# Performance work log

Measured on AMD Instinct MI355X. Metric: run time of the kernel, lower is better.

## Reference

```python
import jax, jax.numpy as jnp
import numpy as np

B, H, D, STEP = 2048, 512, 256, 64  # batch, context_size (cell), thetas_dim (proj/input), steps


def setup_inputs() -> dict:
    key = jax.random.key(0)
    ks = jax.random.split(key, 6)
    s = 1.0 / np.sqrt(H)  # PyTorch LSTM init scale
    c = jax.random.normal(ks[0], (B, H, 1), jnp.float32)
    W_ih = jax.random.uniform(ks[1], (4 * H, D), jnp.float32, -s, s)
    W_hh = jax.random.uniform(ks[2], (4 * H, D), jnp.float32, -s, s)  # hidden input is projected -> dim D
    b_ih = jax.random.uniform(ks[3], (4 * H,), jnp.float32, -s, s)
    b_hh = jax.random.uniform(ks[4], (4 * H,), jnp.float32, -s, s)
    W_hr = jax.random.uniform(ks[5], (D, H), jnp.float32, -s, s)  # projection weight (proj_size=D)
    return {"c": c, "W_ih": W_ih, "W_hh": W_hh, "b_ih": b_ih, "b_hh": b_hh, "W_hr": W_hr, "step": STEP}


def reference(c, W_ih, W_hh, b_ih, b_hh, W_hr, step):
    # c: [batch, hidden, num_layers=1] -> initial cell state [batch, hidden]
    batch = c.shape[0]
    d = W_ih.shape[1]
    c0 = c[:, :, 0]
    h0 = jnp.zeros((batch, d), c.dtype)  # x0 == h0 == 0; thereafter fed-back input x equals projected h

    def cell(carry, _):
        h, cc = carry
        # gates: input term (x==h) + hidden term, PyTorch order i,f,g,o
        z = h @ W_ih.T + b_ih + h @ W_hh.T + b_hh  # [batch, 4H]
        i, f, g, o = jnp.split(z, 4, axis=-1)
        i = jax.nn.sigmoid(i)
        f = jax.nn.sigmoid(f)
        g = jnp.tanh(g)
        o = jax.nn.sigmoid(o)
        cc = f * cc + i * g
        h_new = (o * jnp.tanh(cc)) @ W_hr.T  # projection to proj_size=D
        return (h_new, cc), h_new

    _, ys = jax.lax.scan(cell, (h0, c0), None, length=step)  # ys: [step, batch, D]
    return jnp.transpose(ys, (1, 2, 0))  # [batch, thetas_dim, step]
```

## Files before the change

### kernel.cpp

```cpp
#include <hip/hip_runtime.h>
#include <cstdint>
#include <cstddef>

constexpr int NB  = 2048;
constexpr int NH  = 512;
constexpr int ND  = 256;
constexpr int NT  = 64;
constexpr int N4H = 2048;

typedef __attribute__((ext_vector_type(8))) __bf16 bf16x8;
typedef __attribute__((ext_vector_type(4))) float  f32x4;

__device__ inline unsigned short f2bf_rne(float f) {
    unsigned u = __builtin_bit_cast(unsigned, f);
    unsigned r = (u + 0x7FFFu + ((u >> 16) & 1u)) >> 16;
    return (unsigned short)r;
}
__device__ inline float bf2f(unsigned short h) {
    unsigned u = ((unsigned)h) << 16;
    return __builtin_bit_cast(float, u);
}

__global__ __launch_bounds__(256) void prep_kernel(
    const float* __restrict__ c,   const float* __restrict__ Wih,
    const float* __restrict__ Whh, const float* __restrict__ bih,
    const float* __restrict__ bhh, const float* __restrict__ Whr,
    float* __restrict__ cc, float* __restrict__ bsum,
    unsigned short* __restrict__ WrH,  unsigned short* __restrict__ WrL,
    unsigned short* __restrict__ WhrH, unsigned short* __restrict__ WhrL,
    unsigned short* __restrict__ hH,   unsigned short* __restrict__ hL)
{
    int i = blockIdx.x * 256 + threadIdx.x;
    cc[i] = c[i];
    if (i < N4H) bsum[i] = bih[i] + bhh[i];
    if (i < N4H * ND) {
        int np = i >> 8, k = i & 255;
        int jg = np >> 7, r = np & 127, g = r >> 5, cu = r & 31;
        int src = (g * NH + jg * 32 + cu) * ND + k;
        float w = Wih[src] + Whh[src];
        unsigned short hi = f2bf_rne(w);
        WrH[i] = hi; WrL[i] = f2bf_rne(w - bf2f(hi));
        hH[i] = 0; hL[i] = 0;
    }
    if (i < ND * NH) {
        float w = Whr[i];
        unsigned short hi = f2bf_rne(w);
        WhrH[i] = hi; WhrL[i] = f2bf_rne(w - bf2f(hi));
    }
}

template <int ROWS>
__device__ __forceinline__ void stage_tile(const unsigned short* __restrict__ g,
                                           int row0, int ldgElems, int k0Elems,
                                           char* smem, int ldsOff, int wave, int lane)
{
    constexpr int QN = ROWS / 32;
#pragma unroll
    for (int q = 0; q < QN; ++q) {
        int L   = wave * (ROWS * 32) + q * 1024 + lane * 16;
        int row = L >> 7;
        int kb  = L & 127;
        int kbs = kb ^ ((row & 7) << 4);
        const char* src = (const char*)g +
            (size_t)(row0 + row) * (ldgElems * 2) + k0Elems * 2 + kbs;
        char* dst = smem + ldsOff + wave * (ROWS * 32) + q * 1024;
        __builtin_amdgcn_global_load_lds(
            (const __attribute__((address_space(1))) unsigned int*)src,
            (__attribute__((address_space(3))) unsigned int*)dst,
            16, 0, 0);
    }
}

__device__ __forceinline__ bf16x8 frag_ld(const char* smem, int off, int row, int kb) {
    int kbs = kb ^ ((row & 7) << 4);
    return *(const bf16x8*)(smem + off + row * 128 + kbs);
}

__global__ __launch_bounds__(256) void gates_step(
    const unsigned short* __restrict__ hH, const unsigned short* __restrict__ hL,
    const unsigned short* __restrict__ WrH, const unsigned short* __restrict__ WrL,
    const float* __restrict__ bsum, float* __restrict__ cc,
    unsigned short* __restrict__ aH, unsigned short* __restrict__ aL)
{
    __shared__ char smem[49152];
    constexpr int AsH = 0, AsL = 8192, BsH = 16384, BsL = 32768;

    const int tid  = threadIdx.x;
    const int lane = tid & 63;
    const int wave = tid >> 6;
    const int wr = wave >> 1, wc = wave & 1;
    const int b0 = blockIdx.x * 64;
    const int ny = blockIdx.y;
    const int n0 = ny * 128;

    f32x4 acc[2][4];
#pragma unroll
    for (int mi = 0; mi < 2; ++mi)
#pragma unroll
        for (int ni = 0; ni < 4; ++ni)
            acc[mi][ni] = f32x4{0.f, 0.f, 0.f, 0.f};

    const int lrow = lane & 15;
    const int lk   = (lane >> 4) * 16;

#pragma unroll 1
    for (int ch = 0; ch < 4; ++ch) {
        __syncthreads();
        stage_tile<64> (hH,  b0, ND, ch * 64, smem, AsH, wave, lane);
        stage_tile<64> (hL,  b0, ND, ch * 64, smem, AsL, wave, lane);
        stage_tile<128>(WrH, n0, ND, ch * 64, smem, BsH, wave, lane);
        stage_tile<128>(WrL, n0, ND, ch * 64, smem, BsL, wave, lane);
        __syncthreads();
#pragma unroll
        for (int kk = 0; kk < 2; ++kk) {
            const int kb = kk * 64 + lk;
            bf16x8 aHf[2], aLf[2], bHf[4], bLf[4];
#pragma unroll
            for (int mi = 0; mi < 2; ++mi) {
                int row = wr * 32 + mi * 16 + lrow;
                aHf[mi] = frag_ld(smem, AsH, row, kb);
                aLf[mi] = frag_ld(smem, AsL, row, kb);
            }
#pragma unroll
            for (int ni = 0; ni < 4; ++ni) {
                int row = wc * 64 + ni * 16 + lrow;
                bHf[ni] = frag_ld(smem, BsH, row, kb);
                bLf[ni] = frag_ld(smem, BsL, row, kb);
            }
#pragma unroll
            for (int mi = 0; mi < 2; ++mi)
#pragma unroll
                for (int ni = 0; ni < 4; ++ni) {
                    acc[mi][ni] = __builtin_amdgcn_mfma_f32_16x16x32_bf16(aHf[mi], bHf[ni], acc[mi][ni], 0, 0, 0);
                    acc[mi][ni] = __builtin_amdgcn_mfma_f32_16x16x32_bf16(aHf[mi], bLf[ni], acc[mi][ni], 0, 0, 0);
                    acc[mi][ni] = __builtin_amdgcn_mfma_f32_16x16x32_bf16(aLf[mi], bHf[ni], acc[mi][ni], 0, 0, 0);
                }
        }
    }
    __syncthreads();
    float (*z)[128] = (float(*)[128])smem;
#pragma unroll
    for (int mi = 0; mi < 2; ++mi)
#pragma unroll
        for (int ni = 0; ni < 4; ++ni)
#pragma unroll
            for (int r = 0; r < 4; ++r) {
                int m = wr * 32 + mi * 16 + (lane >> 4) * 4 + r;
                int n = wc * 64 + ni * 16 + (lane & 15);
                z[m][n] = acc[mi][ni][r];
            }
    __syncthreads();
    const int cu = tid & 31;
    const int rg = tid >> 5;
    const int j  = ny * 32 + cu;
    const float bi = bsum[0 * NH + j], bfv = bsum[1 * NH + j];
    const float bg = bsum[2 * NH + j], bo  = bsum[3 * NH + j];
#pragma unroll
    for (int it = 0; it < 8; ++it) {
        int m = rg * 8 + it;
        size_t idx = (size_t)(b0 + m) * NH + j;
        float zi = z[m][cu]      + bi;
        float zf = z[m][32 + cu] + bfv;
        float zg = z[m][64 + cu] + bg;
        float zo = z[m][96 + cu] + bo;
        float iv = 1.f / (1.f + expf(-zi));
        float fv = 1.f / (1.f + expf(-zf));
        float gv = tanhf(zg);
        float ov = 1.f / (1.f + expf(-zo));
        float cv = fv * cc[idx] + iv * gv;
        cc[idx] = cv;
        float av = ov * tanhf(cv);
        unsigned short ah = f2bf_rne(av);
        aH[idx] = ah;
        aL[idx] = f2bf_rne(av - bf2f(ah));
    }
}

template <bool STAGED>
__global__ __launch_bounds__(256) void recur_step(
    const unsigned short* __restrict__ aH, const unsigned short* __restrict__ aL,
    const unsigned short* __restrict__ WhrHp, const unsigned short* __restrict__ WhrLp,
    unsigned short* __restrict__ hH, unsigned short* __restrict__ hL,
    float* __restrict__ hseq, float* __restrict__ out, int t)
{
    __shared__ char smem[16384];
    constexpr int AsH = 0, AsL = 4096, BsH = 8192, BsL = 12288;

    const int tid  = threadIdx.x;
    const int lane = tid & 63;
    const int wave = tid >> 6;
    const int wr = wave >> 1, wc = wave & 1;
    const int b0 = blockIdx.x * 32;
    const int d0 = blockIdx.y * 32;

    f32x4 acc = f32x4{0.f, 0.f, 0.f, 0.f};

    const int lrow = lane & 15;
    const int lk   = (lane >> 4) * 16;

#pragma unroll 1
    for (int ch = 0; ch < 8; ++ch) {
        __syncthreads();
        stage_tile<32>(aH,    b0, NH, ch * 64, smem, AsH, wave, lane);
        stage_tile<32>(aL,    b0, NH, ch * 64, smem, AsL, wave, lane);
        stage_tile<32>(WhrHp, d0, NH, ch * 64, smem, BsH, wave, lane);
        stage_tile<32>(WhrLp, d0, NH, ch * 64, smem, BsL, wave, lane);
        __syncthreads();
#pragma unroll
        for (int kk = 0; kk < 2; ++kk) {
            const int kb = kk * 64 + lk;
            int arow = wr * 16 + lrow;
            int brow = wc * 16 + lrow;
            bf16x8 aHf = frag_ld(smem, AsH, arow, kb);
            bf16x8 aLf = frag_ld(smem, AsL, arow, kb);
            bf16x8 bHf = frag_ld(smem, BsH, brow, kb);
            bf16x8 bLf = frag_ld(smem, BsL, brow, kb);
            acc = __builtin_amdgcn_mfma_f32_16x16x32_bf16(aHf, bHf, acc, 0, 0, 0);
            acc = __builtin_amdgcn_mfma_f32_16x16x32_bf16(aHf, bLf, acc, 0, 0, 0);
            acc = __builtin_amdgcn_mfma_f32_16x16x32_bf16(aLf, bHf, acc, 0, 0, 0);
        }
    }
#pragma unroll
    for (int r = 0; r < 4; ++r) {
        int b = b0 + wr * 16 + (lane >> 4) * 4 + r;
        int d = d0 + wc * 16 + (lane & 15);
        float v = acc[r];
        if (STAGED) hseq[((size_t)t * NB + b) * ND + d] = v;
        else        out[((size_t)b * ND + d) * NT + t]  = v;
        size_t hidx = (size_t)b * ND + d;
        unsigned short hh = f2bf_rne(v);
        hH[hidx] = hh;
        hL[hidx] = f2bf_rne(v - bf2f(hh));
    }
}

__global__ __launch_bounds__(256) void transpose_kernel(
    const float* __restrict__ hseq, float* __restrict__ out) {
    __shared__ float tile[64][65];
    const int tid = threadIdx.x;
    const int d0  = blockIdx.x * 64;
    const int b   = blockIdx.y;
    const int x   = tid & 63;
    const int y   = tid >> 6;
#pragma unroll
    for (int r = 0; r < 16; ++r) {
        int t = y + r * 4;
        tile[t][x] = hseq[((size_t)t * NB + b) * ND + d0 + x];
    }
    __syncthreads();
#pragma unroll
    for (int r = 0; r < 16; ++r) {
        int d = y + r * 4;
        out[((size_t)b * ND + d0 + d) * NT + x] = tile[x][d];
    }
}

extern "C" void kernel_launch(void* const* d_in, const int* in_sizes, int n_in,
                              void* d_out, int out_size, void* d_ws, size_t ws_size,
                              hipStream_t stream) {
    const float* c   = (const float*)d_in[0];
    const float* Wih = (const float*)d_in[1];
    const float* Whh = (const float*)d_in[2];
    const float* bih = (const float*)d_in[3];
    const float* bhh = (const float*)d_in[4];
    const float* Whr = (const float*)d_in[5];
    float* out = (float*)d_out;

    char* ws = (char*)d_ws;
    size_t off = 0;
    auto alloc = [&](size_t bytes) -> char* {
        char* p = ws + off;
        off = (off + bytes + 255) & ~(size_t)255;
        return p;
    };
    float*          cc    = (float*)alloc((size_t)NB * NH * 4);
    float*          bsum  = (float*)alloc((size_t)N4H * 4);
    unsigned short* WrHp  = (unsigned short*)alloc((size_t)N4H * ND * 2);
    unsigned short* WrLp  = (unsigned short*)alloc((size_t)N4H * ND * 2);
    unsigned short* WhrHp = (unsigned short*)alloc((size_t)ND * NH * 2);
    unsigned short* WhrLp = (unsigned short*)alloc((size_t)ND * NH * 2);
    unsigned short* hH    = (unsigned short*)alloc((size_t)NB * ND * 2);
    unsigned short* hL    = (unsigned short*)alloc((size_t)NB * ND * 2);
    unsigned short* aH    = (unsigned short*)alloc((size_t)NB * NH * 2);
    unsigned short* aL    = (unsigned short*)alloc((size_t)NB * NH * 2);
    size_t hseq_bytes = (size_t)NT * NB * ND * 4;
    float* hseq = (float*)(ws + off);
    const bool staged = (off + hseq_bytes) <= ws_size;

    prep_kernel<<<(NB * NH) / 256, 256, 0, stream>>>(
        c, Wih, Whh, bih, bhh, Whr, cc, bsum, WrHp, WrLp, WhrHp, WhrLp, hH, hL);

    dim3 g1(NB / 64, N4H / 128);
    dim3 g2(NB / 32, ND / 32);
    for (int t = 0; t < NT; ++t) {
        gates_step<<<g1, 256, 0, stream>>>(hH, hL, WrHp, WrLp, bsum, cc, aH, aL);
        if (staged)
            recur_step<true><<<g2, 256, 0, stream>>>(aH, aL, WhrHp, WhrLp,
                                                     hH, hL, hseq, out, t);
        else
            recur_step<false><<<g2, 256, 0, stream>>>(aH, aL, WhrHp, WhrLp,
                                                      hH, hL, hseq, out, t);
    }
    if (staged) {
        dim3 gt(ND / 64, NB);
        transpose_kernel<<<gt, 256, 0, stream>>>(hseq, out);
    }
}
```

Measured before the change: 1.504 ms.

## Fold projection weight into gate weights and batch the output projection across steps

Precomputes W_big = (W_ih+W_hh)·W_hr once, so each step's gates are computed directly from the previous step's pre-projection activation. This leaves one kernel per step instead of two. Every step's activation is kept in a sequence buffer, and the projection to the outputs runs once as a single batched GEMM over all steps. The aim is to halve per-step launches and serial dependencies. The cost is that the per-step gate GEMM grows from K=256 to K=512, plus a large activation history buffer.

```diff
diff --git a/kernel.cpp b/kernel.cpp
--- a/kernel.cpp
+++ b/kernel.cpp
@@ -7,6 +7,7 @@
 constexpr int ND  = 256;
 constexpr int NT  = 64;
 constexpr int N4H = 2048;
+constexpr size_t SLOT = (size_t)NB * NH;
 
 typedef __attribute__((ext_vector_type(8))) __bf16 bf16x8;
 typedef __attribute__((ext_vector_type(4))) float  f32x4;
@@ -21,32 +22,87 @@
     return __builtin_bit_cast(float, u);
 }
 
-__global__ __launch_bounds__(256) void prep_kernel(
+__global__ __launch_bounds__(256) void prep1_kernel(
     const float* __restrict__ c,   const float* __restrict__ Wih,
     const float* __restrict__ Whh, const float* __restrict__ bih,
     const float* __restrict__ bhh, const float* __restrict__ Whr,
     float* __restrict__ cc, float* __restrict__ bsum,
-    unsigned short* __restrict__ WrH,  unsigned short* __restrict__ WrL,
+    float* __restrict__ Wsum_reord,
     unsigned short* __restrict__ WhrH, unsigned short* __restrict__ WhrL,
-    unsigned short* __restrict__ hH,   unsigned short* __restrict__ hL)
+    unsigned short* __restrict__ aHseq, unsigned short* __restrict__ aLseq)
 {
     int i = blockIdx.x * 256 + threadIdx.x;
     cc[i] = c[i];
+    aHseq[i] = 0; aLseq[i] = 0;
     if (i < N4H) bsum[i] = bih[i] + bhh[i];
     if (i < N4H * ND) {
         int np = i >> 8, k = i & 255;
         int jg = np >> 7, r = np & 127, g = r >> 5, cu = r & 31;
         int src = (g * NH + jg * 32 + cu) * ND + k;
-        float w = Wih[src] + Whh[src];
-        unsigned short hi = f2bf_rne(w);
-        WrH[i] = hi; WrL[i] = f2bf_rne(w - bf2f(hi));
-        hH[i] = 0; hL[i] = 0;
+        Wsum_reord[i] = Wih[src] + Whh[src];
     }
     if (i < ND * NH) {
         float w = Whr[i];
         unsigned short hi = f2bf_rne(w);
         WhrH[i] = hi; WhrL[i] = f2bf_rne(w - bf2f(hi));
     }
+}
+
+__global__ __launch_bounds__(256) void prep2_kernel(
+    const float* __restrict__ Wsum_reord, const float* __restrict__ Whr,
+    unsigned short* __restrict__ WbigH, unsigned short* __restrict__ WbigL)
+{
+    __shared__ float a_s[64][65];
+    __shared__ float b_s[64][68];
+    const int tid = threadIdx.x;
+    const int n0 = blockIdx.x * 64;
+    const int h0 = blockIdx.y * 64;
+    const int r  = tid >> 2;
+    const int q  = tid & 3;
+    const int tn = (tid & 15) * 4;
+    const int th = (tid >> 4) * 4;
+
+    float acc[4][4] = {};
+#pragma unroll 1
+    for (int ch = 0; ch < 4; ++ch) {
+        __syncthreads();
+#pragma unroll
+        for (int e = 0; e < 4; ++e) {
+            float4 v = *reinterpret_cast<const float4*>(
+                &Wsum_reord[(size_t)(n0 + r) * ND + ch * 64 + q * 16 + e * 4]);
+            int k = q * 16 + e * 4;
+            a_s[k + 0][r] = v.x; a_s[k + 1][r] = v.y;
+            a_s[k + 2][r] = v.z; a_s[k + 3][r] = v.w;
+        }
+#pragma unroll
+        for (int e = 0; e < 4; ++e) {
+            float4 v = *reinterpret_cast<const float4*>(
+                &Whr[(size_t)(ch * 64 + r) * NH + h0 + q * 16 + e * 4]);
+            *reinterpret_cast<float4*>(&b_s[r][q * 16 + e * 4]) = v;
+        }
+        __syncthreads();
+#pragma unroll 8
+        for (int k = 0; k < 64; ++k) {
+            float av[4], bv[4];
+#pragma unroll
+            for (int e = 0; e < 4; ++e) { av[e] = a_s[k][tn + e]; bv[e] = b_s[k][th + e]; }
+#pragma unroll
+            for (int ii = 0; ii < 4; ++ii)
+#pragma unroll
+                for (int jj = 0; jj < 4; ++jj)
+                    acc[ii][jj] += av[ii] * bv[jj];
+        }
+    }
+#pragma unroll
+    for (int ii = 0; ii < 4; ++ii)
+#pragma unroll
+        for (int jj = 0; jj < 4; ++jj) {
+            float w = acc[ii][jj];
+            unsigned short hi = f2bf_rne(w);
+            size_t idx = (size_t)(n0 + tn + ii) * NH + h0 + th + jj;
+            WbigH[idx] = hi;
+            WbigL[idx] = f2bf_rne(w - bf2f(hi));
+        }
 }
 
 template <int ROWS>
@@ -76,15 +132,13 @@
     return *(const bf16x8*)(smem + off + row * 128 + kbs);
 }
 
-__global__ __launch_bounds__(256) void gates_step(
-    const unsigned short* __restrict__ hH, const unsigned short* __restrict__ hL,
-    const unsigned short* __restrict__ WrH, const unsigned short* __restrict__ WrL,
-    const float* __restrict__ bsum, float* __restrict__ cc,
-    unsigned short* __restrict__ aH, unsigned short* __restrict__ aL)
+__global__ __launch_bounds__(256) void step_kernel(
+    const unsigned short* __restrict__ aHseq, const unsigned short* __restrict__ aLseq,
+    const unsigned short* __restrict__ WbigH, const unsigned short* __restrict__ WbigL,
+    const float* __restrict__ bsum, float* __restrict__ cc, int t)
 {
     __shared__ char smem[49152];
     constexpr int AsH = 0, AsL = 8192, BsH = 16384, BsL = 32768;
-
     const int tid  = threadIdx.x;
     const int lane = tid & 63;
     const int wave = tid >> 6;
@@ -93,6 +147,9 @@
     const int ny = blockIdx.y;
     const int n0 = ny * 128;
 
+    const unsigned short* aH = aHseq + (size_t)t * SLOT;
+    const unsigned short* aL = aLseq + (size_t)t * SLOT;
+
     f32x4 acc[2][4];
 #pragma unroll
     for (int mi = 0; mi < 2; ++mi)
@@ -104,12 +161,12 @@
     const int lk   = (lane >> 4) * 16;
 
 #pragma unroll 1
-    for (int ch = 0; ch < 4; ++ch) {
-        __syncthreads();
-        stage_tile<64> (hH,  b0, ND, ch * 64, smem, AsH, wave, lane);
-        stage_tile<64> (hL,  b0, ND, ch * 64, smem, AsL, wave, lane);
-        stage_tile<128>(WrH, n0, ND, ch * 64, smem, BsH, wave, lane);
-        stage_tile<128>(WrL, n0, ND, ch * 64, smem, BsL, wave, lane);
+    for (int ch = 0; ch < 8; ++ch) {
+        __syncthreads();
+        stage_tile<64> (aH,    b0, NH, ch * 64, smem, AsH, wave, lane);
+        stage_tile<64> (aL,    b0, NH, ch * 64, smem, AsL, wave, lane);
+        stage_tile<128>(WbigH, n0, NH, ch * 64, smem, BsH, wave, lane);
+        stage_tile<128>(WbigL, n0, NH, ch * 64, smem, BsL, wave, lane);
         __syncthreads();
 #pragma unroll
         for (int kk = 0; kk < 2; ++kk) {
@@ -155,6 +212,8 @@
     const int j  = ny * 32 + cu;
     const float bi = bsum[0 * NH + j], bfv = bsum[1 * NH + j];
     const float bg = bsum[2 * NH + j], bo  = bsum[3 * NH + j];
+    unsigned short* aHo = (unsigned short*)aHseq + (size_t)(t + 1) * SLOT;
+    unsigned short* aLo = (unsigned short*)aLseq + (size_t)(t + 1) * SLOT;
 #pragma unroll
     for (int it = 0; it < 8; ++it) {
         int m = rg * 8 + it;
@@ -171,29 +230,36 @@
         cc[idx] = cv;
         float av = ov * tanhf(cv);
         unsigned short ah = f2bf_rne(av);
-        aH[idx] = ah;
-        aL[idx] = f2bf_rne(av - bf2f(ah));
-    }
-}
-
-template <bool STAGED>
-__global__ __launch_bounds__(256) void recur_step(
-    const unsigned short* __restrict__ aH, const unsigned short* __restrict__ aL,
-    const unsigned short* __restrict__ WhrHp, const unsigned short* __restrict__ WhrLp,
-    unsigned short* __restrict__ hH, unsigned short* __restrict__ hL,
-    float* __restrict__ hseq, float* __restrict__ out, int t)
-{
-    __shared__ char smem[16384];
-    constexpr int AsH = 0, AsL = 4096, BsH = 8192, BsL = 12288;
-
+        aHo[idx] = ah;
+        aLo[idx] = f2bf_rne(av - bf2f(ah));
+    }
+}
+
+template <bool DIRECT>
+__global__ __launch_bounds__(256) void y_kernel(
+    const unsigned short* __restrict__ aHseq, const unsigned short* __restrict__ aLseq,
+    const unsigned short* __restrict__ WhrH, const unsigned short* __restrict__ WhrL,
+    float* __restrict__ hseq, float* __restrict__ out)
+{
+    __shared__ char smem[49152];
+    constexpr int AsH = 0, AsL = 8192, BsH = 16384, BsL = 32768;
     const int tid  = threadIdx.x;
     const int lane = tid & 63;
     const int wave = tid >> 6;
     const int wr = wave >> 1, wc = wave & 1;
-    const int b0 = blockIdx.x * 32;
-    const int d0 = blockIdx.y * 32;
-
-    f32x4 acc = f32x4{0.f, 0.f, 0.f, 0.f};
+    const int b0 = blockIdx.x * 64;
+    const int d0 = blockIdx.y * 128;
+    const int t  = blockIdx.z;
+
+    const unsigned short* aH = aHseq + (size_t)(t + 1) * SLOT;
+    const unsigned short* aL = aLseq + (size_t)(t + 1) * SLOT;
+
+    f32x4 acc[2][4];
+#pragma unroll
+    for (int mi = 0; mi < 2; ++mi)
+#pragma unroll
+        for (int ni = 0; ni < 4; ++ni)
+            acc[mi][ni] = f32x4{0.f, 0.f, 0.f, 0.f};
 
     const int lrow = lane & 15;
     const int lk   = (lane >> 4) * 16;
@@ -201,37 +267,49 @@
 #pragma unroll 1
     for (int ch = 0; ch < 8; ++ch) {
         __syncthreads();
-        stage_tile<32>(aH,    b0, NH, ch * 64, smem, AsH, wave, lane);
-        stage_tile<32>(aL,    b0, NH, ch * 64, smem, AsL, wave, lane);
-        stage_tile<32>(WhrHp, d0, NH, ch * 64, smem, BsH, wave, lane);
-        stage_tile<32>(WhrLp, d0, NH, ch * 64, smem, BsL, wave, lane);
+        stage_tile<64> (aH,   b0, NH, ch * 64, smem, AsH, wave, lane);
+        stage_tile<64> (aL,   b0, NH, ch * 64, smem, AsL, wave, lane);
+        stage_tile<128>(WhrH, d0, NH, ch * 64, smem, BsH, wave, lane);
+        stage_tile<128>(WhrL, d0, NH, ch * 64, smem, BsL, wave, lane);
         __syncthreads();
 #pragma unroll
         for (int kk = 0; kk < 2; ++kk) {
             const int kb = kk * 64 + lk;
-            int arow = wr * 16 + lrow;
-            int brow = wc * 16 + lrow;
-            bf16x8 aHf = frag_ld(smem, AsH, arow, kb);
-            bf16x8 aLf = frag_ld(smem, AsL, arow, kb);
-            bf16x8 bHf = frag_ld(smem, BsH, brow, kb);
-            bf16x8 bLf = frag_ld(smem, BsL, brow, kb);
-            acc = __builtin_amdgcn_mfma_f32_16x16x32_bf16(aHf, bHf, acc, 0, 0, 0);
-            acc = __builtin_amdgcn_mfma_f32_16x16x32_bf16(aHf, bLf, acc, 0, 0, 0);
-            acc = __builtin_amdgcn_mfma_f32_16x16x32_bf16(aLf, bHf, acc, 0, 0, 0);
-        }
-    }
-#pragma unroll
-    for (int r = 0; r < 4; ++r) {
-        int b = b0 + wr * 16 + (lane >> 4) * 4 + r;
-        int d = d0 + wc * 16 + (lane & 15);
-        float v = acc[r];
-        if (STAGED) hseq[((size_t)t * NB + b) * ND + d] = v;
-        else        out[((size_t)b * ND + d) * NT + t]  = v;
-        size_t hidx = (size_t)b * ND + d;
-        unsigned short hh = f2bf_rne(v);
-        hH[hidx] = hh;
-        hL[hidx] = f2bf_rne(v - bf2f(hh));
-    }
+            bf16x8 aHf[2], aLf[2], bHf[4], bLf[4];
+#pragma unroll
+            for (int mi = 0; mi < 2; ++mi) {
+                int row = wr * 32 + mi * 16 + lrow;
+                aHf[mi] = frag_ld(smem, AsH, row, kb);
+                aLf[mi] = frag_ld(smem, AsL, row, kb);
+            }
+#pragma unroll
+            for (int ni = 0; ni < 4; ++ni) {
+                int row = wc * 64 + ni * 16 + lrow;
+                bHf[ni] = frag_ld(smem, BsH, row, kb);
+                bLf[ni] = frag_ld(smem, BsL, row, kb);
+            }
+#pragma unroll
+            for (int mi = 0; mi < 2; ++mi)
+#pragma unroll
+                for (int ni = 0; ni < 4; ++ni) {
+                    acc[mi][ni] = __builtin_amdgcn_mfma_f32_16x16x32_bf16(aHf[mi], bHf[ni], acc[mi][ni], 0, 0, 0);
+                    acc[mi][ni] = __builtin_amdgcn_mfma_f32_16x16x32_bf16(aHf[mi], bLf[ni], acc[mi][ni], 0, 0, 0);
+                    acc[mi][ni] = __builtin_amdgcn_mfma_f32_16x16x32_bf16(aLf[mi], bHf[ni], acc[mi][ni], 0, 0, 0);
+                }
+        }
+    }
+#pragma unroll
+    for (int mi = 0; mi < 2; ++mi)
+#pragma unroll
+        for (int ni = 0; ni < 4; ++ni)
+#pragma unroll
+            for (int r = 0; r < 4; ++r) {
+                int b = b0 + wr * 32 + mi * 16 + (lane >> 4) * 4 + r;
+                int d = d0 + wc * 64 + ni * 16 + (lane & 15);
+                float v = acc[mi][ni][r];
+                if (DIRECT) out[((size_t)b * ND + d) * NT + t] = v;
+                else        hseq[((size_t)t * NB + b) * ND + d] = v;
+            }
 }
 
 __global__ __launch_bounds__(256) void transpose_kernel(
@@ -273,36 +351,34 @@
         off = (off + bytes + 255) & ~(size_t)255;
         return p;
     };
-    float*          cc    = (float*)alloc((size_t)NB * NH * 4);
-    float*          bsum  = (float*)alloc((size_t)N4H * 4);
-    unsigned short* WrHp  = (unsigned short*)alloc((size_t)N4H * ND * 2);
-    unsigned short* WrLp  = (unsigned short*)alloc((size_t)N4H * ND * 2);
-    unsigned short* WhrHp = (unsigned short*)alloc((size_t)ND * NH * 2);
-    unsigned short* WhrLp = (unsigned short*)alloc((size_t)ND * NH * 2);
-    unsigned short* hH    = (unsigned short*)alloc((size_t)NB * ND * 2);
-    unsigned short* hL    = (unsigned short*)alloc((size_t)NB * ND * 2);
-    unsigned short* aH    = (unsigned short*)alloc((size_t)NB * NH * 2);
-    unsigned short* aL    = (unsigned short*)alloc((size_t)NB * NH * 2);
+    float*          cc     = (float*)alloc((size_t)NB * NH * 4);
+    float*          bsum   = (float*)alloc((size_t)N4H * 4);
+    float*          Wsum_r = (float*)alloc((size_t)N4H * ND * 4);
+    unsigned short* WbigH  = (unsigned short*)alloc((size_t)N4H * NH * 2);
+    unsigned short* WbigL  = (unsigned short*)alloc((size_t)N4H * NH * 2);
+    unsigned short* WhrH   = (unsigned short*)alloc((size_t)ND * NH * 2);
+    unsigned short* WhrL   = (unsigned short*)alloc((size_t)ND * NH * 2);
+    unsigned short* aHseq  = (unsigned short*)alloc((NT + 1) * SLOT * 2);
+    unsigned short* aLseq  = (unsigned short*)alloc((NT + 1) * SLOT * 2);
     size_t hseq_bytes = (size_t)NT * NB * ND * 4;
     float* hseq = (float*)(ws + off);
     const bool staged = (off + hseq_bytes) <= ws_size;
 
-    prep_kernel<<<(NB * NH) / 256, 256, 0, stream>>>(
-        c, Wih, Whh, bih, bhh, Whr, cc, bsum, WrHp, WrLp, WhrHp, WhrLp, hH, hL);
-
-    dim3 g1(NB / 64, N4H / 128);
-    dim3 g2(NB / 32, ND / 32);
-    for (int t = 0; t < NT; ++t) {
-        gates_step<<<g1, 256, 0, stream>>>(hH, hL, WrHp, WrLp, bsum, cc, aH, aL);
-        if (staged)
-            recur_step<true><<<g2, 256, 0, stream>>>(aH, aL, WhrHp, WhrLp,
-                                                     hH, hL, hseq, out, t);
-        else
-            recur_step<false><<<g2, 256, 0, stream>>>(aH, aL, WhrHp, WhrLp,
-                                                      hH, hL, hseq, out, t);
-    }
+    prep1_kernel<<<(NB * NH) / 256, 256, 0, stream>>>(
+        c, Wih, Whh, bih, bhh, Whr, cc, bsum, Wsum_r, WhrH, WhrL, aHseq, aLseq);
+    prep2_kernel<<<dim3(N4H / 64, NH / 64), 256, 0, stream>>>(
+        Wsum_r, Whr, WbigH, WbigL);
+
+    dim3 gs(NB / 64, N4H / 128);
+    for (int t = 0; t < NT; ++t)
+        step_kernel<<<gs, 256, 0, stream>>>(aHseq, aLseq, WbigH, WbigL, bsum, cc, t);
+
+    dim3 gy(NB / 64, ND / 128, NT);
     if (staged) {
+        y_kernel<false><<<gy, 256, 0, stream>>>(aHseq, aLseq, WhrH, WhrL, hseq, out);
         dim3 gt(ND / 64, NB);
         transpose_kernel<<<gt, 256, 0, stream>>>(hseq, out);
-    }
-}
+    } else {
+        y_kernel<true><<<gy, 256, 0, stream>>>(aHseq, aLseq, WhrH, WhrL, hseq, out);
+    }
+}
```

Result: slower. 1.583 ms (+5.2%).
